# Kernel tuning notes

Hardware: AMD Instinct MI355X
Metric: run time of the kernel (lower is better)

The kernel has to match this reference:

```python
import math
import jax, jax.numpy as jnp
import numpy as np

N_FLOWS = 5
DIM = 64
NH = 128          # hidden multiplier -> hidden width = DIM*NH = 8192
BATCH = 4096


def _masks(out_f, in_f, dim):
    od, idd = out_f // dim, in_f // dim
    mask_d = np.zeros((out_f, in_f), np.float32)
    mask_o = np.ones((out_f, in_f), np.float32)
    for i in range(dim):
        mask_d[i * od:(i + 1) * od, i * idd:(i + 1) * idd] = 1.0
        mask_o[i * od:(i + 1) * od, i * idd:] = 0.0
    return jnp.asarray(mask_d), jnp.asarray(mask_o)

MASK_D1, MASK_O1 = _masks(DIM * NH, DIM, DIM)   # layer 1: (H, D)
MASK_D2, MASK_O2 = _masks(DIM, DIM * NH, DIM)   # layer 2: (D, H)


def masked_weight(x, W, dw, b, mask_d, mask_o, dim, grad=None):
    """MaskedWeight.forward. W:(out,in), dw:(out,1), b:(out,)."""
    out_f, in_f = W.shape
    od, idd = out_f // dim, in_f // dim
    w = jnp.exp(W) * mask_d + W * mask_o                 # (out, in)
    wsn = jnp.sum(w * w, axis=-1, keepdims=True)         # (out, 1)
    wn = jnp.exp(dw) * w / jnp.sqrt(wsn)                 # weight-normalized
    wpl = dw + W - 0.5 * jnp.log(wsn)                    # (out, in)
    # extract diagonal blocks of wpl^T: (dim, idd, od)
    blocks = wpl.reshape(dim, od, dim, idd)
    wpl_t = blocks[np.arange(dim), :, np.arange(dim), :].transpose(0, 2, 1)
    y = x @ wn.T + b                                     # (B, out)
    g = wpl_t.transpose(0, 2, 1)                         # (dim, od, idd)
    if grad is None:
        new_grad = jnp.broadcast_to(g[None], (x.shape[0],) + g.shape)
    else:
        # logsumexp over contracted block axis: out (B, dim, od, b_prev)
        new_grad = jax.nn.logsumexp(
            g[None, :, :, None, :] + jnp.swapaxes(grad, -2, -1)[:, :, None, :, :],
            axis=-1)
    return y, new_grad


def tanh_layer(x, grad):
    g = -2.0 * (x - math.log(2.0) + jax.nn.softplus(-2.0 * x))
    return jnp.tanh(x), g.reshape(grad.shape) + grad


def bnaf_flow(x, W1, d1, b1, W2, d2, b2, gate):
    h, g = masked_weight(x, W1, d1, b1, MASK_D1, MASK_O1, DIM)
    h, g = tanh_layer(h, g)
    y, g = masked_weight(h, W2, d2, b2, MASK_D2, MASK_O2, DIM, grad=g)
    grad = g[:, :, 0, 0]                                  # (B, DIM) -- squeeze
    if gate is None:                                      # res=None (last flow)
        return y, jnp.sum(grad, axis=-1)
    s = jax.nn.sigmoid(gate)                              # res='gated'
    out = s * y + (1.0 - s) * x
    ld = jnp.sum(jax.nn.softplus(grad + gate) - jax.nn.softplus(gate), axis=-1)
    return out, ld


def setup_inputs() -> dict:
    key = jax.random.key(0)
    ks = jax.random.split(key, 8)
    H = DIM * NH
    return {
        "x":  jax.random.normal(ks[0], (BATCH, DIM), jnp.float32),
        "W1": jax.random.normal(ks[1], (N_FLOWS, H, DIM), jnp.float32) * 0.1,
        "d1": jax.random.normal(ks[2], (N_FLOWS, H, 1), jnp.float32) * 0.1,
        "b1": jax.random.normal(ks[3], (N_FLOWS, H), jnp.float32) * 0.01,
        "W2": jax.random.normal(ks[4], (N_FLOWS, DIM, H), jnp.float32) * 0.1,
        "d2": jax.random.normal(ks[5], (N_FLOWS, DIM, 1), jnp.float32) * 0.1,
        "b2": jax.random.normal(ks[6], (N_FLOWS, DIM), jnp.float32) * 0.01,
        "gates": jax.random.normal(ks[7], (N_FLOWS - 1,), jnp.float32),
    }


def reference(x, W1, d1, b1, W2, d2, b2, gates):
    log_det = jnp.zeros(x.shape[0], x.dtype)
    for f in range(N_FLOWS):
        gate = gates[f] if f < N_FLOWS - 1 else None
        x, ld = bnaf_flow(x, W1[f], d1[f], b1[f], W2[f], d2[f], b2[f], gate)
        log_det = log_det + ld
        if f < N_FLOWS - 1:                               # Permutation 'flip'
            x = x[:, ::-1]
    return x, log_det
```

## Files before the change

### kernel.cpp

```cpp
#include <hip/hip_runtime.h>
#include <hip/hip_bf16.h>
#include <math.h>

#define NFLOWS 5
#define DIMF 64
#define HID 8192
#define BATCHN 4096

typedef unsigned int u32;
typedef __bf16 bf16x8 __attribute__((ext_vector_type(8)));
typedef float f32x4 __attribute__((ext_vector_type(4)));

__device__ __forceinline__ short f2bf_s(float x){
  u32 b = __float_as_uint(x);
  b += 0x7fff + ((b >> 16) & 1);
  return (short)(b >> 16);
}
__device__ __forceinline__ u32 pk_bf16(float a, float b){
#if __has_builtin(__builtin_amdgcn_cvt_pk_bf16_f32)
  typedef __bf16 bf16x2_t __attribute__((ext_vector_type(2)));
  bf16x2_t r = __builtin_amdgcn_cvt_pk_bf16_f32(a, b);
  return __builtin_bit_cast(u32, r);
#else
  u32 x = __float_as_uint(a); x += 0x7fff + ((x >> 16) & 1);
  u32 y = __float_as_uint(b); y += 0x7fff + ((y >> 16) & 1);
  return (x >> 16) | (y & 0xffff0000u);
#endif
}
__device__ __forceinline__ float softplus_f(float z){
  return fmaxf(z, 0.f) + log1pf(__expf(-fabsf(z)));
}

__global__ __launch_bounds__(256) void prep1_kernel(
    const float* __restrict__ W1, const float* __restrict__ d1,
    short* __restrict__ wn1s, float* __restrict__ g1)
{
  int w = threadIdx.x >> 6;
  int k = threadIdx.x & 63;
  int R = blockIdx.x * 4 + w;
  int rl = R & (HID - 1);
  int blk = rl >> 7;
  float Wv = W1[(size_t)R * DIMF + k];
  float wv;
  if (k == blk)      wv = __expf(Wv);
  else if (k < blk)  wv = Wv;
  else               wv = 0.f;
  float sq = wv * wv;
  #pragma unroll
  for (int m = 1; m < 64; m <<= 1) sq += __shfl_xor(sq, m, 64);
  float d1v = d1[R];
  float sc = __expf(d1v) * rsqrtf(sq);
  int f   = R >> 13;
  int i   = rl >> 7;
  int rem = rl & 127;
  int nt  = rem >> 4;
  int n16 = rem & 15;
  int ks2 = k >> 5;
  int q   = (k & 31) >> 3;
  int j   = k & 7;
  size_t dst = ((((size_t)(f * 64 + i) * 8 + nt) * 2 + ks2) << 9)
             + ((q * 16 + n16) << 3) + j;
  wn1s[dst] = f2bf_s(wv * sc);
  if (k == blk) g1[R] = d1v + Wv - 0.5f * __logf(sq);
}

__global__ __launch_bounds__(256) void prep2_kernel(
    const float* __restrict__ W2, const float* __restrict__ d2,
    const float* __restrict__ g1,
    short* __restrict__ wn2s, float* __restrict__ expc4,
    float* __restrict__ cmax)
{
  int wid  = blockIdx.x * 4 + (threadIdx.x >> 6);
  int lane = threadIdx.x & 63;
  int f = wid >> 6, iRow = wid & 63;
  const float* Wrow = W2 + ((size_t)(f * DIMF + iRow)) * HID;
  float d2v = d2[f * DIMF + iRow];
  int mt2 = iRow >> 4, c16r = iRow & 15;

  float p0 = 0.f, p1 = 0.f;
  #pragma unroll 4
  for (int it = 0; it < 16; ++it) {
    int k0 = it * 512 + lane * 8;
    int kb = k0 >> 7;
    float4 a = *(const float4*)(Wrow + k0);
    float4 b = *(const float4*)(Wrow + k0 + 4);
    float wv[8] = {a.x, a.y, a.z, a.w, b.x, b.y, b.z, b.w};
    if (kb == iRow) {
      #pragma unroll
      for (int e = 0; e < 8; ++e) wv[e] = __expf(wv[e]);
    } else if (kb > iRow) {
      #pragma unroll
      for (int e = 0; e < 8; ++e) wv[e] = 0.f;
    }
    p0 += wv[0]*wv[0] + wv[1]*wv[1] + wv[2]*wv[2] + wv[3]*wv[3];
    p1 += wv[4]*wv[4] + wv[5]*wv[5] + wv[6]*wv[6] + wv[7]*wv[7];
  }
  float part = p0 + p1;
  #pragma unroll
  for (int m = 1; m < 64; m <<= 1) part += __shfl_xor(part, m, 64);
  float ls = __logf(part);
  float sc = __expf(d2v) * rsqrtf(part);

  float cvr[8]; int k0d = -1; float lm = -1e30f;
  #pragma unroll 4
  for (int it = 0; it < 16; ++it) {
    int k0 = it * 512 + lane * 8;
    int kb = k0 >> 7;
    float4 a = *(const float4*)(Wrow + k0);
    float4 b = *(const float4*)(Wrow + k0 + 4);
    float wv[8] = {a.x, a.y, a.z, a.w, b.x, b.y, b.z, b.w};
    if (kb == iRow) {
      float4 ga = *(const float4*)(g1 + f * HID + k0);
      float4 gb = *(const float4*)(g1 + f * HID + k0 + 4);
      float gg[8] = {ga.x, ga.y, ga.z, ga.w, gb.x, gb.y, gb.z, gb.w};
      #pragma unroll
      for (int e = 0; e < 8; ++e) {
        cvr[e] = gg[e] + d2v + wv[e] - 0.5f * ls;
        lm = fmaxf(lm, cvr[e]);
        wv[e] = __expf(wv[e]);
      }
      k0d = k0;
    } else if (kb > iRow) {
      #pragma unroll
      for (int e = 0; e < 8; ++e) wv[e] = 0.f;
    }
    int i = k0 >> 7, ks = (k0 >> 5) & 3, qq = (k0 >> 3) & 3;
    size_t dst = ((((size_t)(f * 64 + i) * 4 + ks) * 4 + mt2) << 9)
               + ((qq * 16 + c16r) << 3);
    uint4 pk4;
    pk4.x = pk_bf16(wv[0]*sc, wv[1]*sc); pk4.y = pk_bf16(wv[2]*sc, wv[3]*sc);
    pk4.z = pk_bf16(wv[4]*sc, wv[5]*sc); pk4.w = pk_bf16(wv[6]*sc, wv[7]*sc);
    *(uint4*)(wn2s + dst) = pk4;
  }
  #pragma unroll
  for (int m = 1; m < 64; m <<= 1) lm = fmaxf(lm, __shfl_xor(lm, m, 64));
  if (k0d >= 0) {
    float4 ea, eb;
    ea.x = 4.f*__expf(cvr[0]-lm); ea.y = 4.f*__expf(cvr[1]-lm);
    ea.z = 4.f*__expf(cvr[2]-lm); ea.w = 4.f*__expf(cvr[3]-lm);
    eb.x = 4.f*__expf(cvr[4]-lm); eb.y = 4.f*__expf(cvr[5]-lm);
    eb.z = 4.f*__expf(cvr[6]-lm); eb.w = 4.f*__expf(cvr[7]-lm);
    *(float4*)(expc4 + f * HID + k0d)     = ea;
    *(float4*)(expc4 + f * HID + k0d + 4) = eb;
  }
  if (lane == 0) cmax[f * DIMF + iRow] = lm;
}

__global__ __launch_bounds__(1024, 4)
void bnaf_main_kernel(
    const float* __restrict__ x_in,
    const float* __restrict__ b1, const float* __restrict__ b2,
    const float* __restrict__ gates,
    const short* __restrict__ wn1s,
    const short* __restrict__ wn2s,
    const float* __restrict__ expc4, const float* __restrict__ cmax,
    float* __restrict__ out)
{
  __shared__ __attribute__((aligned(16))) char smem[146816];
  float* xs  = (float*)smem;
  short* xbS = (short*)(smem + 4352);
  float* ldp = (float*)(smem + 145792);

  const int tid  = threadIdx.x;
  const int w    = tid >> 6;
  const int lane = tid & 63;
  const int c16  = lane & 15;
  const int q    = lane >> 4;
  const int r0   = blockIdx.x * 16;

  short* tbuf0 = (short*)(smem + 6528 + w * 8704);
  short* tbuf1 = (short*)(smem + 6528 + w * 8704 + 4352);

  {
    int row = tid >> 6, col = tid & 63;
    float v = x_in[((size_t)(r0 + row) << 6) | col];
    xs[row * 68 + col] = v;
    xbS[(col >> 3) * 136 + row * 8 + (col & 7)] = f2bf_s(v);
  }
  float ldtot = 0.f;
  __syncthreads();

  #pragma unroll 1
  for (int f = 0; f < NFLOWS; ++f) {
    const float gatev = (f < NFLOWS - 1) ? gates[f] : 0.f;
    const float spg   = (f < NFLOWS - 1) ? softplus_f(gatev) : 0.f;

    const bf16x8 xa0 = *(const bf16x8*)(xbS + q * 136 + c16 * 8);
    const bf16x8 xa1 = *(const bf16x8*)(xbS + (4 + q) * 136 + c16 * 8);

    f32x4 yacc[4];
    #pragma unroll
    for (int n = 0; n < 4; ++n) yacc[n] = f32x4{0.f, 0.f, 0.f, 0.f};
    float ldacc = 0.f;

    #pragma unroll 1
    for (int ii = 0; ii < 4; ++ii) {
      const int i = ii * 16 + w;
      short* tb = (ii & 1) ? tbuf1 : tbuf0;
      const short* p1l = wn1s + (((size_t)(f * 64 + i)) << 13) + lane * 8;
      const float* b1p = b1    + f * HID + i * 128 + q * 4;
      const float* ecp = expc4 + f * HID + i * 128 + q * 4;
      const bool hiHalf = (i >= 32);

      float s0 = 0.f, s1 = 0.f;
      f32x4 dd[4];

      #pragma unroll
      for (int nt = 0; nt < 4; ++nt) {
        float4 b1q = *(const float4*)(b1p + nt * 16);
        f32x4 z = {b1q.x, b1q.y, b1q.z, b1q.w};
        bf16x8 bw0 = *(const bf16x8*)(p1l + nt * 1024);
        dd[nt] = __builtin_amdgcn_mfma_f32_16x16x32_bf16(bw0, xa0, z, 0, 0, 0);
      }
      if (hiHalf) {
        #pragma unroll
        for (int nt = 0; nt < 4; ++nt) {
          bf16x8 bw1 = *(const bf16x8*)(p1l + nt * 1024 + 512);
          dd[nt] = __builtin_amdgcn_mfma_f32_16x16x32_bf16(bw1, xa1, dd[nt], 0, 0, 0);
        }
      }
      #pragma unroll
      for (int nt = 0; nt < 4; ++nt) {
        float4 ecq = *(const float4*)(ecp + nt * 16);
        float t[4];
        #pragma unroll
        for (int r = 0; r < 4; ++r) {
          float ee = (r == 0) ? ecq.x : (r == 1) ? ecq.y : (r == 2) ? ecq.z : ecq.w;
          float h  = dd[nt][r];
          float up = __expf(-2.f * fabsf(h));
          float vp = __builtin_amdgcn_rcpf(1.f + up);
          float ta = fmaf(-2.f * up, vp, 1.f);
          t[r] = copysignf(ta, h);
          float c1 = ee * up, c2 = vp * vp;
          if (r & 1) s1 = fmaf(c1, c2, s1); else s0 = fmaf(c1, c2, s0);
        }
        uint2 pk; pk.x = pk_bf16(t[0], t[1]); pk.y = pk_bf16(t[2], t[3]);
        *(uint2*)(tb + c16 * 136 + nt * 16 + q * 4) = pk;
      }

      if (ii > 0) {
        const int ip = i - 16;
        short* tp = ((ii - 1) & 1) ? tbuf1 : tbuf0;
        asm volatile("s_waitcnt lgkmcnt(0)" ::: "memory");
        const short* p2l = wn2s + (((size_t)(f * 64 + ip)) << 13) + lane * 8;
        const int mt0 = ip >> 4;
        #pragma unroll
        for (int ks = 0; ks < 4; ++ks) {
          bf16x8 tfrag = *(const bf16x8*)(tp + c16 * 136 + ks * 32 + q * 8);
          #pragma unroll
          for (int mt = 0; mt < 4; ++mt) {
            if (mt >= mt0) {
              bf16x8 wb = *(const bf16x8*)(p2l + (ks * 4 + mt) * 512);
              yacc[mt] = __builtin_amdgcn_mfma_f32_16x16x32_bf16(wb, tfrag, yacc[mt], 0, 0, 0);
            }
          }
        }
      }

      #pragma unroll
      for (int nt = 0; nt < 4; ++nt) {
        float4 b1q = *(const float4*)(b1p + (nt + 4) * 16);
        f32x4 z = {b1q.x, b1q.y, b1q.z, b1q.w};
        bf16x8 bw0 = *(const bf16x8*)(p1l + (nt + 4) * 1024);
        dd[nt] = __builtin_amdgcn_mfma_f32_16x16x32_bf16(bw0, xa0, z, 0, 0, 0);
      }
      if (hiHalf) {
        #pragma unroll
        for (int nt = 0; nt < 4; ++nt) {
          bf16x8 bw1 = *(const bf16x8*)(p1l + (nt + 4) * 1024 + 512);
          dd[nt] = __builtin_amdgcn_mfma_f32_16x16x32_bf16(bw1, xa1, dd[nt], 0, 0, 0);
        }
      }
      #pragma unroll
      for (int nt = 0; nt < 4; ++nt) {
        float4 ecq = *(const float4*)(ecp + (nt + 4) * 16);
        float t[4];
        #pragma unroll
        for (int r = 0; r < 4; ++r) {
          float ee = (r == 0) ? ecq.x : (r == 1) ? ecq.y : (r == 2) ? ecq.z : ecq.w;
          float h  = dd[nt][r];
          float up = __expf(-2.f * fabsf(h));
          float vp = __builtin_amdgcn_rcpf(1.f + up);
          float ta = fmaf(-2.f * up, vp, 1.f);
          t[r] = copysignf(ta, h);
          float c1 = ee * up, c2 = vp * vp;
          if (r & 1) s1 = fmaf(c1, c2, s1); else s0 = fmaf(c1, c2, s0);
        }
        uint2 pk; pk.x = pk_bf16(t[0], t[1]); pk.y = pk_bf16(t[2], t[3]);
        *(uint2*)(tb + c16 * 136 + (nt + 4) * 16 + q * 4) = pk;
      }

      float sacc = s0 + s1;
      sacc += __shfl_xor(sacc, 16, 64);
      sacc += __shfl_xor(sacc, 32, 64);
      const float Mi = cmax[f * DIMF + i];
      float grad = Mi + __logf(sacc);
      ldacc += (f < NFLOWS - 1) ? (softplus_f(grad + gatev) - spg) : grad;
    }

    {
      const int ip = 48 + w;
      asm volatile("s_waitcnt lgkmcnt(0)" ::: "memory");
      const short* p2l = wn2s + (((size_t)(f * 64 + ip)) << 13) + lane * 8;
      const int mt0 = ip >> 4;
      #pragma unroll
      for (int ks = 0; ks < 4; ++ks) {
        bf16x8 tfrag = *(const bf16x8*)(tbuf1 + c16 * 136 + ks * 32 + q * 8);
        #pragma unroll
        for (int mt = 0; mt < 4; ++mt) {
          if (mt >= mt0) {
            bf16x8 wb = *(const bf16x8*)(p2l + (ks * 4 + mt) * 512);
            yacc[mt] = __builtin_amdgcn_mfma_f32_16x16x32_bf16(wb, tfrag, yacc[mt], 0, 0, 0);
          }
        }
      }
    }

    float* ypw = (float*)(smem + 6528 + w * 8704);
    #pragma unroll
    for (int mt = 0; mt < 4; ++mt)
      #pragma unroll
      for (int r = 0; r < 4; ++r)
        ypw[(mt * 4 + r) * 65 + lane] = yacc[mt][r];
    if (q == 0) ldp[w * 16 + c16] = ldacc;
    __syncthreads();

    float sgate = 0.f;
    if (f < NFLOWS - 1) sgate = __builtin_amdgcn_rcpf(1.f + __expf(-gatev));
    int row = tid >> 6, col = tid & 63;
    int idx = ((col >> 4) * 4 + (col & 3)) * 65 + (((col >> 2) & 3) * 16 + row);
    float v = b2[f * DIMF + col];
    #pragma unroll
    for (int ww = 0; ww < 16; ++ww)
      v += ((const float*)(smem + 6528 + ww * 8704))[idx];
    float nx = 0.f; int nrow = 0, ncol = 0;
    if (f < NFLOWS - 1) {
      float xv = xs[row * 68 + col];
      nx = fmaf(sgate, v - xv, xv);
      nrow = row; ncol = 63 - col;
    } else {
      out[((size_t)(r0 + row) << 6) | col] = v;
    }
    if (tid < 16) {
      float a = 0.f;
      #pragma unroll
      for (int ww = 0; ww < 16; ++ww) a += ldp[ww * 16 + tid];
      ldtot += a;
    }
    __syncthreads();
    if (f < NFLOWS - 1) {
      xs[nrow * 68 + ncol] = nx;
      xbS[(ncol >> 3) * 136 + nrow * 8 + (ncol & 7)] = f2bf_s(nx);
      __syncthreads();
    }
  }

  if (tid < 16) out[(size_t)BATCHN * DIMF + r0 + tid] = ldtot;
}

extern "C" void kernel_launch(void* const* d_in, const int* in_sizes, int n_in,
                              void* d_out, int out_size, void* d_ws, size_t ws_size,
                              hipStream_t stream)
{
  const float* x     = (const float*)d_in[0];
  const float* W1    = (const float*)d_in[1];
  const float* d1    = (const float*)d_in[2];
  const float* b1    = (const float*)d_in[3];
  const float* W2    = (const float*)d_in[4];
  const float* d2    = (const float*)d_in[5];
  const float* b2    = (const float*)d_in[6];
  const float* gates = (const float*)d_in[7];
  float* out = (float*)d_out;

  char* ws = (char*)d_ws;
  short* wn1s  = (short*)ws;
  short* wn2s  = (short*)(ws + 5242880);
  float* expc4 = (float*)(ws + 10485760);
  float* cmaxp = (float*)(ws + 10649600);
  float* g1    = (float*)(ws + 10650880);

  hipLaunchKernelGGL(prep1_kernel, dim3(10240), dim3(256), 0, stream, W1, d1, wn1s, g1);
  hipLaunchKernelGGL(prep2_kernel, dim3(80), dim3(256), 0, stream, W2, d2, g1, wn2s, expc4, cmaxp);
  hipLaunchKernelGGL(bnaf_main_kernel, dim3(256), dim3(1024), 0, stream,
                     x, b1, b2, gates, wn1s, wn2s, expc4, cmaxp, out);
}
```

Measured before the change: 267.8 us.

## Fuse weight-prep kernels and interleave bias with gradient constants

Merges the two weight-preparation kernels into one kernel with a block per (flow, diagonal block) pair. The W1 log-diagonal values and the logsumexp constants stay in shared memory instead of going through global memory, and one launch is saved. The prep for W2 now runs on 320 blocks of 256 threads instead of 80 blocks of four row-per-wave groups, which gives it more parallelism. In the main kernel, b1 and the exp constants are interleaved into one float2 array so each tile needs one stream of loads, and the bias is added after the MFMA instead of seeding the accumulator. The x fragments are reloaded from LDS per tile, which may lower register pressure.

```diff
diff --git a/kernel.cpp b/kernel.cpp
--- a/kernel.cpp
+++ b/kernel.cpp
@@ -31,129 +31,130 @@
   return fmaxf(z, 0.f) + log1pf(__expf(-fabsf(z)));
 }
 
-__global__ __launch_bounds__(256) void prep1_kernel(
+__global__ __launch_bounds__(256) void prep_fused_kernel(
     const float* __restrict__ W1, const float* __restrict__ d1,
-    short* __restrict__ wn1s, float* __restrict__ g1)
+    const float* __restrict__ b1,
+    const float* __restrict__ W2, const float* __restrict__ d2,
+    short* __restrict__ wn1s, short* __restrict__ wn2s,
+    float* __restrict__ bec, float* __restrict__ cmax)
 {
-  int w = threadIdx.x >> 6;
-  int k = threadIdx.x & 63;
-  int R = blockIdx.x * 4 + w;
-  int rl = R & (HID - 1);
-  int blk = rl >> 7;
-  float Wv = W1[(size_t)R * DIMF + k];
-  float wv;
-  if (k == blk)      wv = __expf(Wv);
-  else if (k < blk)  wv = Wv;
-  else               wv = 0.f;
-  float sq = wv * wv;
+  __shared__ float g1s[128];
+  __shared__ float cbuf[128];
+  __shared__ float red[4];
+  __shared__ float Msh;
+
+  const int tid  = threadIdx.x;
+  const int w    = tid >> 6;
+  const int lane = tid & 63;
+  const int f    = blockIdx.x >> 6;
+  const int i    = blockIdx.x & 63;
+
+  {
+    const int ks2 = lane >> 5, q = (lane & 31) >> 3, j = lane & 7;
+    #pragma unroll 4
+    for (int it = 0; it < 32; ++it) {
+      int rr = w * 32 + it;
+      size_t R = (size_t)(f * HID + i * 128 + rr);
+      float Wv = W1[R * 64 + lane];
+      float wv = (lane == i) ? __expf(Wv) : ((lane < i) ? Wv : 0.f);
+      float sq = wv * wv;
+      #pragma unroll
+      for (int m = 1; m < 64; m <<= 1) sq += __shfl_xor(sq, m, 64);
+      float d1v = d1[R];
+      float sc = __expf(d1v) * rsqrtf(sq);
+      int nt = rr >> 4, n16 = rr & 15;
+      size_t dst = ((((size_t)(f * 64 + i) * 8 + nt) * 2 + ks2) << 9)
+                 + ((q * 16 + n16) << 3) + j;
+      wn1s[dst] = f2bf_s(wv * sc);
+      if (lane == i) g1s[rr] = d1v + Wv - 0.5f * __logf(sq);
+    }
+  }
+  __syncthreads();
+
+  const float* Wrow = W2 + ((size_t)(f * DIMF + i)) * HID;
+  const float d2v = d2[f * DIMF + i];
+
+  float part = 0.f;
   #pragma unroll
-  for (int m = 1; m < 64; m <<= 1) sq += __shfl_xor(sq, m, 64);
-  float d1v = d1[R];
-  float sc = __expf(d1v) * rsqrtf(sq);
-  int f   = R >> 13;
-  int i   = rl >> 7;
-  int rem = rl & 127;
-  int nt  = rem >> 4;
-  int n16 = rem & 15;
-  int ks2 = k >> 5;
-  int q   = (k & 31) >> 3;
-  int j   = k & 7;
-  size_t dst = ((((size_t)(f * 64 + i) * 8 + nt) * 2 + ks2) << 9)
-             + ((q * 16 + n16) << 3) + j;
-  wn1s[dst] = f2bf_s(wv * sc);
-  if (k == blk) g1[R] = d1v + Wv - 0.5f * __logf(sq);
-}
-
-__global__ __launch_bounds__(256) void prep2_kernel(
-    const float* __restrict__ W2, const float* __restrict__ d2,
-    const float* __restrict__ g1,
-    short* __restrict__ wn2s, float* __restrict__ expc4,
-    float* __restrict__ cmax)
-{
-  int wid  = blockIdx.x * 4 + (threadIdx.x >> 6);
-  int lane = threadIdx.x & 63;
-  int f = wid >> 6, iRow = wid & 63;
-  const float* Wrow = W2 + ((size_t)(f * DIMF + iRow)) * HID;
-  float d2v = d2[f * DIMF + iRow];
-  int mt2 = iRow >> 4, c16r = iRow & 15;
-
-  float p0 = 0.f, p1 = 0.f;
-  #pragma unroll 4
-  for (int it = 0; it < 16; ++it) {
-    int k0 = it * 512 + lane * 8;
+  for (int it = 0; it < 4; ++it) {
+    int k0 = it * 2048 + tid * 8;
     int kb = k0 >> 7;
     float4 a = *(const float4*)(Wrow + k0);
     float4 b = *(const float4*)(Wrow + k0 + 4);
     float wv[8] = {a.x, a.y, a.z, a.w, b.x, b.y, b.z, b.w};
-    if (kb == iRow) {
+    if (kb == i) {
       #pragma unroll
       for (int e = 0; e < 8; ++e) wv[e] = __expf(wv[e]);
-    } else if (kb > iRow) {
+    } else if (kb > i) {
       #pragma unroll
       for (int e = 0; e < 8; ++e) wv[e] = 0.f;
     }
-    p0 += wv[0]*wv[0] + wv[1]*wv[1] + wv[2]*wv[2] + wv[3]*wv[3];
-    p1 += wv[4]*wv[4] + wv[5]*wv[5] + wv[6]*wv[6] + wv[7]*wv[7];
-  }
-  float part = p0 + p1;
+    #pragma unroll
+    for (int e = 0; e < 8; ++e) part = fmaf(wv[e], wv[e], part);
+  }
   #pragma unroll
   for (int m = 1; m < 64; m <<= 1) part += __shfl_xor(part, m, 64);
-  float ls = __logf(part);
-  float sc = __expf(d2v) * rsqrtf(part);
-
-  float cvr[8]; int k0d = -1; float lm = -1e30f;
-  #pragma unroll 4
-  for (int it = 0; it < 16; ++it) {
-    int k0 = it * 512 + lane * 8;
+  if (lane == 0) red[w] = part;
+  __syncthreads();
+  float wsn = red[0] + red[1] + red[2] + red[3];
+  float ls = __logf(wsn);
+  float sc = __expf(d2v) * rsqrtf(wsn);
+
+  const int mt2 = i >> 4, c16r = i & 15;
+  #pragma unroll
+  for (int it = 0; it < 4; ++it) {
+    int k0 = it * 2048 + tid * 8;
     int kb = k0 >> 7;
     float4 a = *(const float4*)(Wrow + k0);
     float4 b = *(const float4*)(Wrow + k0 + 4);
     float wv[8] = {a.x, a.y, a.z, a.w, b.x, b.y, b.z, b.w};
-    if (kb == iRow) {
-      float4 ga = *(const float4*)(g1 + f * HID + k0);
-      float4 gb = *(const float4*)(g1 + f * HID + k0 + 4);
-      float gg[8] = {ga.x, ga.y, ga.z, ga.w, gb.x, gb.y, gb.z, gb.w};
+    if (kb == i) {
+      int rr0 = k0 - i * 128;
       #pragma unroll
       for (int e = 0; e < 8; ++e) {
-        cvr[e] = gg[e] + d2v + wv[e] - 0.5f * ls;
-        lm = fmaxf(lm, cvr[e]);
+        cbuf[rr0 + e] = g1s[rr0 + e] + d2v + wv[e] - 0.5f * ls;
         wv[e] = __expf(wv[e]);
       }
-      k0d = k0;
-    } else if (kb > iRow) {
+    } else if (kb > i) {
       #pragma unroll
       for (int e = 0; e < 8; ++e) wv[e] = 0.f;
     }
-    int i = k0 >> 7, ks = (k0 >> 5) & 3, qq = (k0 >> 3) & 3;
-    size_t dst = ((((size_t)(f * 64 + i) * 4 + ks) * 4 + mt2) << 9)
+    int ib = k0 >> 7, ks = (k0 >> 5) & 3, qq = (k0 >> 3) & 3;
+    size_t dst = ((((size_t)(f * 64 + ib) * 4 + ks) * 4 + mt2) << 9)
                + ((qq * 16 + c16r) << 3);
     uint4 pk4;
     pk4.x = pk_bf16(wv[0]*sc, wv[1]*sc); pk4.y = pk_bf16(wv[2]*sc, wv[3]*sc);
     pk4.z = pk_bf16(wv[4]*sc, wv[5]*sc); pk4.w = pk_bf16(wv[6]*sc, wv[7]*sc);
     *(uint4*)(wn2s + dst) = pk4;
   }
-  #pragma unroll
-  for (int m = 1; m < 64; m <<= 1) lm = fmaxf(lm, __shfl_xor(lm, m, 64));
-  if (k0d >= 0) {
-    float4 ea, eb;
-    ea.x = 4.f*__expf(cvr[0]-lm); ea.y = 4.f*__expf(cvr[1]-lm);
-    ea.z = 4.f*__expf(cvr[2]-lm); ea.w = 4.f*__expf(cvr[3]-lm);
-    eb.x = 4.f*__expf(cvr[4]-lm); eb.y = 4.f*__expf(cvr[5]-lm);
-    eb.z = 4.f*__expf(cvr[6]-lm); eb.w = 4.f*__expf(cvr[7]-lm);
-    *(float4*)(expc4 + f * HID + k0d)     = ea;
-    *(float4*)(expc4 + f * HID + k0d + 4) = eb;
-  }
-  if (lane == 0) cmax[f * DIMF + iRow] = lm;
+  __syncthreads();
+
+  if (w == 0) {
+    float m = fmaxf(cbuf[lane], cbuf[lane + 64]);
+    #pragma unroll
+    for (int s = 1; s < 64; s <<= 1) m = fmaxf(m, __shfl_xor(m, s, 64));
+    if (lane == 0) { cmax[f * DIMF + i] = m; Msh = m; }
+  }
+  __syncthreads();
+  float M = Msh;
+
+  if (tid < 128) {
+    int k = i * 128 + tid;
+    float2 v;
+    v.x = b1[f * HID + k];
+    v.y = 4.f * __expf(cbuf[tid] - M);
+    *(float2*)(bec + (((size_t)(f * HID + k)) << 1)) = v;
+  }
 }
 
 __global__ __launch_bounds__(1024, 4)
 void bnaf_main_kernel(
     const float* __restrict__ x_in,
-    const float* __restrict__ b1, const float* __restrict__ b2,
+    const float* __restrict__ b2,
     const float* __restrict__ gates,
     const short* __restrict__ wn1s,
     const short* __restrict__ wn2s,
-    const float* __restrict__ expc4, const float* __restrict__ cmax,
+    const float* __restrict__ bec, const float* __restrict__ cmax,
     float* __restrict__ out)
 {
   __shared__ __attribute__((aligned(16))) char smem[146816];
@@ -185,9 +186,6 @@
     const float gatev = (f < NFLOWS - 1) ? gates[f] : 0.f;
     const float spg   = (f < NFLOWS - 1) ? softplus_f(gatev) : 0.f;
 
-    const bf16x8 xa0 = *(const bf16x8*)(xbS + q * 136 + c16 * 8);
-    const bf16x8 xa1 = *(const bf16x8*)(xbS + (4 + q) * 136 + c16 * 8);
-
     f32x4 yacc[4];
     #pragma unroll
     for (int n = 0; n < 4; ++n) yacc[n] = f32x4{0.f, 0.f, 0.f, 0.f};
@@ -198,35 +196,39 @@
       const int i = ii * 16 + w;
       short* tb = (ii & 1) ? tbuf1 : tbuf0;
       const short* p1l = wn1s + (((size_t)(f * 64 + i)) << 13) + lane * 8;
-      const float* b1p = b1    + f * HID + i * 128 + q * 4;
-      const float* ecp = expc4 + f * HID + i * 128 + q * 4;
+      const float* becp = bec + (((size_t)(f * HID + i * 128 + q * 4)) << 1);
       const bool hiHalf = (i >= 32);
 
       float s0 = 0.f, s1 = 0.f;
       f32x4 dd[4];
 
+      {
+        const bf16x8 xa0 = *(const bf16x8*)(xbS + q * 136 + c16 * 8);
+        #pragma unroll
+        for (int nt = 0; nt < 4; ++nt) {
+          f32x4 z = {0.f, 0.f, 0.f, 0.f};
+          bf16x8 bw0 = *(const bf16x8*)(p1l + nt * 1024);
+          dd[nt] = __builtin_amdgcn_mfma_f32_16x16x32_bf16(bw0, xa0, z, 0, 0, 0);
+        }
+        if (hiHalf) {
+          const bf16x8 xa1 = *(const bf16x8*)(xbS + (4 + q) * 136 + c16 * 8);
+          #pragma unroll
+          for (int nt = 0; nt < 4; ++nt) {
+            bf16x8 bw1 = *(const bf16x8*)(p1l + nt * 1024 + 512);
+            dd[nt] = __builtin_amdgcn_mfma_f32_16x16x32_bf16(bw1, xa1, dd[nt], 0, 0, 0);
+          }
+        }
+      }
       #pragma unroll
       for (int nt = 0; nt < 4; ++nt) {
-        float4 b1q = *(const float4*)(b1p + nt * 16);
-        f32x4 z = {b1q.x, b1q.y, b1q.z, b1q.w};
-        bf16x8 bw0 = *(const bf16x8*)(p1l + nt * 1024);
-        dd[nt] = __builtin_amdgcn_mfma_f32_16x16x32_bf16(bw0, xa0, z, 0, 0, 0);
-      }
-      if (hiHalf) {
-        #pragma unroll
-        for (int nt = 0; nt < 4; ++nt) {
-          bf16x8 bw1 = *(const bf16x8*)(p1l + nt * 1024 + 512);
-          dd[nt] = __builtin_amdgcn_mfma_f32_16x16x32_bf16(bw1, xa1, dd[nt], 0, 0, 0);
-        }
-      }
-      #pragma unroll
-      for (int nt = 0; nt < 4; ++nt) {
-        float4 ecq = *(const float4*)(ecp + nt * 16);
+        float4 e0 = *(const float4*)(becp + nt * 32);
+        float4 e1 = *(const float4*)(becp + nt * 32 + 4);
         float t[4];
         #pragma unroll
         for (int r = 0; r < 4; ++r) {
-          float ee = (r == 0) ? ecq.x : (r == 1) ? ecq.y : (r == 2) ? ecq.z : ecq.w;
-          float h  = dd[nt][r];
+          float bb = (r == 0) ? e0.x : (r == 1) ? e0.z : (r == 2) ? e1.x : e1.z;
+          float ee = (r == 0) ? e0.y : (r == 1) ? e0.w : (r == 2) ? e1.y : e1.w;
+          float h  = dd[nt][r] + bb;
           float up = __expf(-2.f * fabsf(h));
           float vp = __builtin_amdgcn_rcpf(1.f + up);
           float ta = fmaf(-2.f * up, vp, 1.f);
@@ -257,28 +259,33 @@
         }
       }
 
+      {
+        const bf16x8 xa0 = *(const bf16x8*)(xbS + q * 136 + c16 * 8);
+        #pragma unroll
+        for (int nt = 0; nt < 4; ++nt) {
+          f32x4 z = {0.f, 0.f, 0.f, 0.f};
+          bf16x8 bw0 = *(const bf16x8*)(p1l + (nt + 4) * 1024);
+          dd[nt] = __builtin_amdgcn_mfma_f32_16x16x32_bf16(bw0, xa0, z, 0, 0, 0);
+        }
+        if (hiHalf) {
+          const bf16x8 xa1 = *(const bf16x8*)(xbS + (4 + q) * 136 + c16 * 8);
+          #pragma unroll
+          for (int nt = 0; nt < 4; ++nt) {
+            bf16x8 bw1 = *(const bf16x8*)(p1l + (nt + 4) * 1024 + 512);
+            dd[nt] = __builtin_amdgcn_mfma_f32_16x16x32_bf16(bw1, xa1, dd[nt], 0, 0, 0);
+          }
+        }
+      }
       #pragma unroll
       for (int nt = 0; nt < 4; ++nt) {
-        float4 b1q = *(const float4*)(b1p + (nt + 4) * 16);
-        f32x4 z = {b1q.x, b1q.y, b1q.z, b1q.w};
-        bf16x8 bw0 = *(const bf16x8*)(p1l + (nt + 4) * 1024);
-        dd[nt] = __builtin_amdgcn_mfma_f32_16x16x32_bf16(bw0, xa0, z, 0, 0, 0);
-      }
-      if (hiHalf) {
-        #pragma unroll
-        for (int nt = 0; nt < 4; ++nt) {
-          bf16x8 bw1 = *(const bf16x8*)(p1l + (nt + 4) * 1024 + 512);
-          dd[nt] = __builtin_amdgcn_mfma_f32_16x16x32_bf16(bw1, xa1, dd[nt], 0, 0, 0);
-        }
-      }
-      #pragma unroll
-      for (int nt = 0; nt < 4; ++nt) {
-        float4 ecq = *(const float4*)(ecp + (nt + 4) * 16);
+        float4 e0 = *(const float4*)(becp + (nt + 4) * 32);
+        float4 e1 = *(const float4*)(becp + (nt + 4) * 32 + 4);
         float t[4];
         #pragma unroll
         for (int r = 0; r < 4; ++r) {
-          float ee = (r == 0) ? ecq.x : (r == 1) ? ecq.y : (r == 2) ? ecq.z : ecq.w;
-          float h  = dd[nt][r];
+          float bb = (r == 0) ? e0.x : (r == 1) ? e0.z : (r == 2) ? e1.x : e1.z;
+          float ee = (r == 0) ? e0.y : (r == 1) ? e0.w : (r == 2) ? e1.y : e1.w;
+          float h  = dd[nt][r] + bb;
           float up = __expf(-2.f * fabsf(h));
           float vp = __builtin_amdgcn_rcpf(1.f + up);
           float ta = fmaf(-2.f * up, vp, 1.f);
@@ -375,12 +382,11 @@
   char* ws = (char*)d_ws;
   short* wn1s  = (short*)ws;
   short* wn2s  = (short*)(ws + 5242880);
-  float* expc4 = (float*)(ws + 10485760);
-  float* cmaxp = (float*)(ws + 10649600);
-  float* g1    = (float*)(ws + 10650880);
-
-  hipLaunchKernelGGL(prep1_kernel, dim3(10240), dim3(256), 0, stream, W1, d1, wn1s, g1);
-  hipLaunchKernelGGL(prep2_kernel, dim3(80), dim3(256), 0, stream, W2, d2, g1, wn2s, expc4, cmaxp);
+  float* bec   = (float*)(ws + 10485760);
+  float* cmaxp = (float*)(ws + 10813440);
+
+  hipLaunchKernelGGL(prep_fused_kernel, dim3(320), dim3(256), 0, stream,
+                     W1, d1, b1, W2, d2, wn1s, wn2s, bec, cmaxp);
   hipLaunchKernelGGL(bnaf_main_kernel, dim3(256), dim3(1024), 0, stream,
-                     x, b1, b2, gates, wn1s, wn2s, expc4, cmaxp, out);
-}
+                     x, b2, gates, wn1s, wn2s, bec, cmaxp, out);
+}
```

Result: slower. 322.3 us (+20.3%).
